# Kernel optimization log

Measured on AMD Instinct MI355X. Metric: run time of the kernel, lower is better.

Reference implementation:

```python
import jax, jax.numpy as jnp
import numpy as np

N = 8192
D_IN = 60
NUM_CLASSES = 10


def _xavier(key, out_f, in_f):
    limit = float(np.sqrt(6.0 / (in_f + out_f)))
    return jax.random.uniform(key, (out_f, in_f), jnp.float32, -limit, limit)


def setup_inputs() -> dict:
    key = jax.random.key(0)
    ks = jax.random.split(key, 10)
    return {
        "x": jax.random.normal(ks[0], (N, D_IN), jnp.float32),
        "fc1_w": _xavier(ks[1], 32, 60),
        "fc1_b": jnp.zeros((32,), jnp.float32),
        "fc2_w": _xavier(ks[2], 16, 32),
        "fc2_b": jnp.zeros((16,), jnp.float32),
        "fc3_w": _xavier(ks[3], 8, 60),
        "fc3_b": jnp.zeros((8,), jnp.float32),
        "fc6_w": _xavier(ks[4], NUM_CLASSES, 8),
        "fc6_b": jnp.zeros((NUM_CLASSES,), jnp.float32),
        "temp": jnp.float32(1.0) + 0.1 * jax.random.truncated_normal(ks[5], -2.0, 2.0, (), jnp.float32),
        "theta": jnp.float32(1.0) + 0.1 * jax.random.truncated_normal(ks[6], -2.0, 2.0, (), jnp.float32),
    }


def _pairwise_sq_dist(z):
    # z: [N, d] -> [N, N] squared euclidean distances, clamped at 0
    sq = jnp.sum(z * z, axis=1)  # [N]
    dist = sq[:, None] + sq[None, :] - 2.0 * (z @ z.T)
    return jnp.maximum(dist, 0.0)


def reference(x, fc1_w, fc1_b, fc2_w, fc2_b, fc3_w, fc3_b, fc6_w, fc6_b, temp, theta):
    net = x @ fc1_w.T + fc1_b           # [N, 32]
    net = net @ fc2_w.T + fc2_b         # [N, 16]
    A = -_pairwise_sq_dist(net)         # [N, N]
    A = jax.nn.sigmoid(temp * A + theta)
    # A * (1 - I) + I == set diagonal to 1
    A = jnp.fill_diagonal(A, 1.0, inplace=False)
    A = A / jnp.sum(A, axis=1, keepdims=True)
    h = A @ x                           # [N, 60] dense graph aggregation
    h = h @ fc3_w.T + fc3_b             # [N, 8]
    return jax.nn.softmax(h @ fc6_w.T + fc6_b, axis=1)  # [N, num_classes]
```

## Files before the change

### kernel.cpp

```cpp
#include <hip/hip_runtime.h>
#include <math.h>

#define NROWS 8192
#define DIN   60
#define DZ    16
#define NC    10

#define LOG2E 1.4426950408889634f

#define RB    64
#define CJ    512
#define NRB   (NROWS / RB)
#define NCH   (NROWS / CJ)
#define WAVES 4

typedef short bf16x8 __attribute__((ext_vector_type(8)));
typedef float f32x4  __attribute__((ext_vector_type(4)));

__device__ __forceinline__ unsigned int bfr(float f) {
    return (__float_as_uint(f) + 0x8000u) >> 16;
}

__global__ __launch_bounds__(64) void k1_all(
    const float* __restrict__ x,
    const float* __restrict__ w1, const float* __restrict__ b1,
    const float* __restrict__ w2, const float* __restrict__ b2,
    const float* __restrict__ temp_p, const float* __restrict__ theta_p,
    unsigned short* __restrict__ zb, float* __restrict__ bbf,
    unsigned short* __restrict__ xT)
{
    int i = blockIdx.x * 64 + threadIdx.x;

    float xr[DIN];
    const float4* xp = reinterpret_cast<const float4*>(x + (size_t)i * DIN);
    #pragma unroll
    for (int c = 0; c < 15; ++c) {
        float4 v = xp[c];
        xr[c*4+0] = v.x; xr[c*4+1] = v.y; xr[c*4+2] = v.z; xr[c*4+3] = v.w;
    }

    float n1[32];
    #pragma unroll
    for (int o = 0; o < 32; ++o) {
        float acc = b1[o];
        #pragma unroll
        for (int k = 0; k < DIN; ++k) acc = fmaf(w1[o*DIN+k], xr[k], acc);
        n1[o] = acc;
    }

    float z[DZ];
    float sq = 0.0f;
    #pragma unroll
    for (int u = 0; u < DZ; ++u) {
        float acc = b2[u];
        #pragma unroll
        for (int o = 0; o < 32; ++o) acc = fmaf(w2[u*32+o], n1[o], acc);
        z[u] = acc;
        sq = fmaf(acc, acc, sq);
    }

    float temp  = *temp_p;
    float theta = *theta_p;
    float s = sqrtf(2.0f * temp * LOG2E);

    unsigned int p[8];
    #pragma unroll
    for (int u = 0; u < 8; ++u) {
        unsigned int lo = bfr(z[2*u]   * s);
        unsigned int hi = bfr(z[2*u+1] * s);
        p[u] = lo | (hi << 16);
    }
    uint4* dst = reinterpret_cast<uint4*>(zb + (size_t)i * 32);
    dst[0] = make_uint4(p[0], p[1], p[2], p[3]);
    dst[1] = make_uint4(p[4], p[5], p[6], p[7]);
    dst[2] = make_uint4(0, 0, 0, 0);
    dst[3] = make_uint4(0, 0, 0, 0);

    bbf[i] = LOG2E * fmaf(temp, sq, -0.5f * theta);

    #pragma unroll
    for (int c = 0; c < DIN; ++c)
        xT[(size_t)c * NROWS + i] = (unsigned short)bfr(xr[c]);
    xT[(size_t)60 * NROWS + i] = 0x3F80;
    xT[(size_t)61 * NROWS + i] = 0;
    xT[(size_t)62 * NROWS + i] = 0;
    xT[(size_t)63 * NROWS + i] = 0;
}

__global__ __launch_bounds__(256, 8) void k2_mfma(
    const unsigned short* __restrict__ zb, const float* __restrict__ bbf,
    const unsigned short* __restrict__ xT, const float* __restrict__ theta_p,
    float* __restrict__ hacc)
{
    __shared__ unsigned long long sP[WAVES * 160];

    const int tid  = threadIdx.x;
    const int lane = tid & 63, wave = tid >> 6;
    const int q = lane & 15, g = lane >> 4;
    const int rb = blockIdx.x & (NRB - 1);
    const int ch = blockIdx.x >> 7;
    const int i0 = rb * RB + wave * 16;
    const int j0 = ch * CJ;

    bf16x8 zbi = *reinterpret_cast<const bf16x8*>(zb + (size_t)(i0 + q) * 32 + g*8);
    float  bi  = bbf[i0 + q];
    const float nclamp = -(*theta_p) * LOG2E;
    const f32x4 z4 = {0.0f, 0.0f, 0.0f, 0.0f};

    f32x4 H[4];
    #pragma unroll
    for (int nt = 0; nt < 4; ++nt) H[nt] = z4;

    unsigned long long* myP = sP + wave * 160;

    for (int jp = 0; jp < CJ / 32; ++jp) {
        #pragma unroll
        for (int half = 0; half < 2; ++half) {
            const int gj = j0 + jp*32 + half*16;
            bf16x8 za = *reinterpret_cast<const bf16x8*>(zb + (size_t)(gj + q) * 32 + g*8);
            f32x4  bj = *reinterpret_cast<const f32x4*>(bbf + gj + 4*g);
            f32x4 S = __builtin_amdgcn_mfma_f32_16x16x32_bf16(za, zbi, z4, 0, 0, 0);
            unsigned int ur[4];
            #pragma unroll
            for (int r = 0; r < 4; ++r) {
                float n = (bi + bj[r]) - S[r];
                n = fmaxf(n, nclamp);
                float P = __builtin_amdgcn_rcpf(1.0f + __builtin_amdgcn_exp2f(n));
                if (i0 == gj && q == 4*g + r) P = 0.0f;
                ur[r] = __float_as_uint(P) + 0x8000u;
            }
            unsigned int pk0 = (ur[0] >> 16) | (ur[1] & 0xFFFF0000u);
            unsigned int pk1 = (ur[2] >> 16) | (ur[3] & 0xFFFF0000u);
            myP[q*10 + half*4 + g] = ((unsigned long long)pk1 << 32) | pk0;
        }
        __threadfence_block();

        const int jb = j0 + jp*32;
        bf16x8 pa;
        {
            union { unsigned long long u[2]; bf16x8 v; } pu;
            pu.u[0] = myP[q*10 + g*2];
            pu.u[1] = myP[q*10 + g*2 + 1];
            pa = pu.v;
        }
        #pragma unroll
        for (int nt = 0; nt < 4; ++nt) {
            bf16x8 xb = *reinterpret_cast<const bf16x8*>(
                xT + (size_t)(nt*16 + q) * NROWS + jb + g*8);
            H[nt] = __builtin_amdgcn_mfma_f32_16x16x32_bf16(pa, xb, H[nt], 0, 0, 0);
        }
    }

    float* regout = hacc + (((size_t)(ch * NRB + rb) * WAVES + wave) * 16) * 64;
    #pragma unroll
    for (int nt = 0; nt < 4; ++nt)
        #pragma unroll
        for (int r = 0; r < 4; ++r)
            regout[(nt*4 + r) * 64 + lane] = H[nt][r];
}

__global__ __launch_bounds__(256) void k3_fused(
    const float* __restrict__ hacc,
    const float* __restrict__ x,
    const float* __restrict__ w3, const float* __restrict__ b3,
    const float* __restrict__ w6, const float* __restrict__ b6,
    float* __restrict__ out)
{
    __shared__ float sh[16][64];

    const int tid = threadIdx.x;
    const int b   = blockIdx.x;

    {
        const float4* src = reinterpret_cast<const float4*>(
            hacc + (size_t)b * 1024) + tid;
        float4 s = make_float4(0.0f, 0.0f, 0.0f, 0.0f);
        #pragma unroll 8
        for (int ch = 0; ch < NCH; ++ch) {
            float4 v = src[(size_t)ch * (NRB * WAVES * 16 * 64 / 4)];
            s.x += v.x; s.y += v.y; s.z += v.z; s.w += v.w;
        }
        const int f    = tid * 4;
        const int lane = f & 63;
        const int slot = (f >> 6) & 15;
        const int il   = (lane >> 4) * 4 + (slot & 3);
        const int cl   = ((slot >> 2) & 3) * 16 + (lane & 15);
        *reinterpret_cast<float4*>(&sh[il][cl]) = s;
    }
    __syncthreads();

    if (tid < 16) {
        const int row = b * 16 + tid;
        const float* hi = sh[tid];
        const float* xi = x + (size_t)row * DIN;

        float rd = __builtin_amdgcn_rcpf(hi[60] + 1.0f);

        float h[DIN];
        #pragma unroll
        for (int k = 0; k < DIN; ++k) h[k] = (hi[k] + xi[k]) * rd;

        float g[8];
        #pragma unroll
        for (int o = 0; o < 8; ++o) {
            float a = b3[o];
            #pragma unroll
            for (int k = 0; k < DIN; ++k) a = fmaf(w3[o*DIN+k], h[k], a);
            g[o] = a;
        }

        float l[NC];
        float m = -3.0e38f;
        #pragma unroll
        for (int c = 0; c < NC; ++c) {
            float a = b6[c];
            #pragma unroll
            for (int o = 0; o < 8; ++o) a = fmaf(w6[c*8+o], g[o], a);
            l[c] = a;
            m = fmaxf(m, a);
        }
        float e[NC];
        float sum = 0.0f;
        #pragma unroll
        for (int c = 0; c < NC; ++c) {
            e[c] = __builtin_amdgcn_exp2f((l[c] - m) * LOG2E);
            sum += e[c];
        }
        float rsum = __builtin_amdgcn_rcpf(sum);
        #pragma unroll
        for (int c = 0; c < NC; ++c) out[(size_t)row * NC + c] = e[c] * rsum;
    }
}

extern "C" void kernel_launch(void* const* d_in, const int* in_sizes, int n_in,
                              void* d_out, int out_size, void* d_ws, size_t ws_size,
                              hipStream_t stream)
{
    const float* x     = (const float*)d_in[0];
    const float* w1    = (const float*)d_in[1];
    const float* b1    = (const float*)d_in[2];
    const float* w2    = (const float*)d_in[3];
    const float* b2    = (const float*)d_in[4];
    const float* w3    = (const float*)d_in[5];
    const float* b3    = (const float*)d_in[6];
    const float* w6    = (const float*)d_in[7];
    const float* b6    = (const float*)d_in[8];
    const float* temp  = (const float*)d_in[9];
    const float* theta = (const float*)d_in[10];
    float* out = (float*)d_out;

    char* p = (char*)d_ws;
    unsigned short* zbuf = (unsigned short*)p;  p += (size_t)NROWS * 32 * 2;
    float*          bbf  = (float*)p;           p += (size_t)NROWS * 4;
    unsigned short* xT   = (unsigned short*)p;  p += (size_t)64 * NROWS * 2;
    float*          hacc = (float*)p;

    k1_all  <<<NROWS / 64, 64, 0, stream>>>(x, w1, b1, w2, b2, temp, theta, zbuf, bbf, xT);
    k2_mfma <<<NRB * NCH, 256, 0, stream>>>(zbuf, bbf, xT, theta, hacc);
    k3_fused<<<NROWS / 16, 256, 0, stream>>>(hacc, x, w3, b3, w6, b6, out);
}
```

Measured before the change: 208.5 us.

## Switch pairwise-similarity kernel to 32x32x16 MFMA with permlane32 register repacking

Moves the distance and aggregation MFMAs from 16x16x32 to 32x32x16 bf16 tiles, with 32 rows per wave and 128 rows per block. The P tile is transposed in registers with permlane32_swap instead of a shared-memory round trip and block fence. The z buffer drops its zero padding from 32 to 16 elements per row. The partial-sum layout is padded per chunk, and k3 is remapped to it with a staggered chunk order. This cuts LDS traffic and raises MFMA work per instruction, in exchange for more accumulator registers and no occupancy hint in launch bounds.

```diff
diff --git a/kernel.cpp b/kernel.cpp
--- a/kernel.cpp
+++ b/kernel.cpp
@@ -8,14 +8,19 @@
 
 #define LOG2E 1.4426950408889634f
 
-#define RB    64
-#define CJ    512
-#define NRB   (NROWS / RB)
-#define NCH   (NROWS / CJ)
-#define WAVES 4
-
-typedef short bf16x8 __attribute__((ext_vector_type(8)));
-typedef float f32x4  __attribute__((ext_vector_type(4)));
+#define RB      128
+#define CJ      512
+#define NRB     (NROWS / RB)
+#define NCH     (NROWS / CJ)
+#define WAVES   4
+#define REGIONS (NRB * WAVES)
+
+#define CHPAD (NROWS * 64 + 1024)
+
+typedef short    bf16x8 __attribute__((ext_vector_type(8)));
+typedef float    f32x4  __attribute__((ext_vector_type(4)));
+typedef float    f32x16 __attribute__((ext_vector_type(16)));
+typedef unsigned u32x2  __attribute__((ext_vector_type(2)));
 
 __device__ __forceinline__ unsigned int bfr(float f) {
     return (__float_as_uint(f) + 0x8000u) >> 16;
@@ -70,11 +75,9 @@
         unsigned int hi = bfr(z[2*u+1] * s);
         p[u] = lo | (hi << 16);
     }
-    uint4* dst = reinterpret_cast<uint4*>(zb + (size_t)i * 32);
+    uint4* dst = reinterpret_cast<uint4*>(zb + (size_t)i * 16);
     dst[0] = make_uint4(p[0], p[1], p[2], p[3]);
     dst[1] = make_uint4(p[4], p[5], p[6], p[7]);
-    dst[2] = make_uint4(0, 0, 0, 0);
-    dst[3] = make_uint4(0, 0, 0, 0);
 
     bbf[i] = LOG2E * fmaf(temp, sq, -0.5f * theta);
 
@@ -87,76 +90,91 @@
     xT[(size_t)63 * NROWS + i] = 0;
 }
 
-__global__ __launch_bounds__(256, 8) void k2_mfma(
+__global__ __launch_bounds__(256) void k2_mfma(
     const unsigned short* __restrict__ zb, const float* __restrict__ bbf,
     const unsigned short* __restrict__ xT, const float* __restrict__ theta_p,
     float* __restrict__ hacc)
 {
-    __shared__ unsigned long long sP[WAVES * 160];
-
     const int tid  = threadIdx.x;
     const int lane = tid & 63, wave = tid >> 6;
-    const int q = lane & 15, g = lane >> 4;
+    const int ic = lane & 31;
+    const int h  = lane >> 5;
     const int rb = blockIdx.x & (NRB - 1);
-    const int ch = blockIdx.x >> 7;
-    const int i0 = rb * RB + wave * 16;
+    const int ch = blockIdx.x >> 6;
+    const int it = rb * RB + wave * 32;
     const int j0 = ch * CJ;
 
-    bf16x8 zbi = *reinterpret_cast<const bf16x8*>(zb + (size_t)(i0 + q) * 32 + g*8);
-    float  bi  = bbf[i0 + q];
+    bf16x8 zbi = *reinterpret_cast<const bf16x8*>(zb + (size_t)(it + ic) * 16 + h * 8);
+    const float bi = bbf[it + ic];
     const float nclamp = -(*theta_p) * LOG2E;
-    const f32x4 z4 = {0.0f, 0.0f, 0.0f, 0.0f};
-
-    f32x4 H[4];
-    #pragma unroll
-    for (int nt = 0; nt < 4; ++nt) H[nt] = z4;
-
-    unsigned long long* myP = sP + wave * 160;
-
-    for (int jp = 0; jp < CJ / 32; ++jp) {
-        #pragma unroll
-        for (int half = 0; half < 2; ++half) {
-            const int gj = j0 + jp*32 + half*16;
-            bf16x8 za = *reinterpret_cast<const bf16x8*>(zb + (size_t)(gj + q) * 32 + g*8);
-            f32x4  bj = *reinterpret_cast<const f32x4*>(bbf + gj + 4*g);
-            f32x4 S = __builtin_amdgcn_mfma_f32_16x16x32_bf16(za, zbi, z4, 0, 0, 0);
-            unsigned int ur[4];
+
+    const int  dd   = ic - 4 * h;
+    const bool dl   = (dd >= 0) && ((dd & 7) < 4);
+    const int  dreg = dl ? (((dd >> 3) << 2) | (dd & 3)) : -1;
+
+    f32x16 z16;
+    #pragma unroll
+    for (int k = 0; k < 16; ++k) z16[k] = 0.0f;
+    f32x16 H0 = z16, H1 = z16;
+
+    for (int jb = 0; jb < CJ / 32; ++jb) {
+        const int jt = j0 + jb * 32;
+        bf16x8 za = *reinterpret_cast<const bf16x8*>(zb + (size_t)(jt + ic) * 16 + h * 8);
+        f32x16 S = __builtin_amdgcn_mfma_f32_32x32x16_bf16(za, zbi, z16, 0, 0, 0);
+
+        const bool dblk = (it == jt);
+        unsigned pk[8];
+        #pragma unroll
+        for (int u = 0; u < 4; ++u) {
+            f32x4 bj = *reinterpret_cast<const f32x4*>(bbf + jt + u * 8 + 4 * h);
+            unsigned ur[4];
             #pragma unroll
             for (int r = 0; r < 4; ++r) {
-                float n = (bi + bj[r]) - S[r];
+                const int reg = u * 4 + r;
+                float n = (bi + bj[r]) - S[reg];
                 n = fmaxf(n, nclamp);
                 float P = __builtin_amdgcn_rcpf(1.0f + __builtin_amdgcn_exp2f(n));
-                if (i0 == gj && q == 4*g + r) P = 0.0f;
+                if (dblk && reg == dreg) P = 0.0f;
                 ur[r] = __float_as_uint(P) + 0x8000u;
             }
-            unsigned int pk0 = (ur[0] >> 16) | (ur[1] & 0xFFFF0000u);
-            unsigned int pk1 = (ur[2] >> 16) | (ur[3] & 0xFFFF0000u);
-            myP[q*10 + half*4 + g] = ((unsigned long long)pk1 << 32) | pk0;
-        }
-        __threadfence_block();
-
-        const int jb = j0 + jp*32;
-        bf16x8 pa;
+            pk[u*2 + 0] = (ur[0] >> 16) | (ur[1] & 0xFFFF0000u);
+            pk[u*2 + 1] = (ur[2] >> 16) | (ur[3] & 0xFFFF0000u);
+        }
+
+        u32x2 sA = __builtin_amdgcn_permlane32_swap(pk[0], pk[2], false, false);
+        u32x2 sB = __builtin_amdgcn_permlane32_swap(pk[1], pk[3], false, false);
+        u32x2 sC = __builtin_amdgcn_permlane32_swap(pk[4], pk[6], false, false);
+        u32x2 sD = __builtin_amdgcn_permlane32_swap(pk[5], pk[7], false, false);
+        union { unsigned u[4]; bf16x8 v; } pa0, pa1;
+        pa0.u[0] = sA[0]; pa0.u[1] = sB[0]; pa0.u[2] = sA[1]; pa0.u[3] = sB[1];
+        pa1.u[0] = sC[0]; pa1.u[1] = sD[0]; pa1.u[2] = sC[1]; pa1.u[3] = sD[1];
+
         {
-            union { unsigned long long u[2]; bf16x8 v; } pu;
-            pu.u[0] = myP[q*10 + g*2];
-            pu.u[1] = myP[q*10 + g*2 + 1];
-            pa = pu.v;
-        }
-        #pragma unroll
-        for (int nt = 0; nt < 4; ++nt) {
-            bf16x8 xb = *reinterpret_cast<const bf16x8*>(
-                xT + (size_t)(nt*16 + q) * NROWS + jb + g*8);
-            H[nt] = __builtin_amdgcn_mfma_f32_16x16x32_bf16(pa, xb, H[nt], 0, 0, 0);
-        }
-    }
-
-    float* regout = hacc + (((size_t)(ch * NRB + rb) * WAVES + wave) * 16) * 64;
-    #pragma unroll
-    for (int nt = 0; nt < 4; ++nt)
-        #pragma unroll
-        for (int r = 0; r < 4; ++r)
-            regout[(nt*4 + r) * 64 + lane] = H[nt][r];
+            bf16x8 xb0 = *reinterpret_cast<const bf16x8*>(
+                xT + (size_t)(ic) * NROWS + jt + h*8);
+            bf16x8 xb1 = *reinterpret_cast<const bf16x8*>(
+                xT + (size_t)(ic) * NROWS + jt + 16 + h*8);
+            H0 = __builtin_amdgcn_mfma_f32_32x32x16_bf16(pa0.v, xb0, H0, 0, 0, 0);
+            H0 = __builtin_amdgcn_mfma_f32_32x32x16_bf16(pa1.v, xb1, H0, 0, 0, 0);
+        }
+        {
+            bf16x8 xb0 = *reinterpret_cast<const bf16x8*>(
+                xT + (size_t)(32 + ic) * NROWS + jt + h*8);
+            bf16x8 xb1 = *reinterpret_cast<const bf16x8*>(
+                xT + (size_t)(32 + ic) * NROWS + jt + 16 + h*8);
+            H1 = __builtin_amdgcn_mfma_f32_32x32x16_bf16(pa0.v, xb0, H1, 0, 0, 0);
+            H1 = __builtin_amdgcn_mfma_f32_32x32x16_bf16(pa1.v, xb1, H1, 0, 0, 0);
+        }
+    }
+
+    const int region = rb * WAVES + wave;
+    float* outp = hacc + (size_t)ch * CHPAD + (size_t)region * 2048;
+    #pragma unroll
+    for (int reg = 0; reg < 16; ++reg)
+        outp[reg * 64 + lane] = H0[reg];
+    #pragma unroll
+    for (int reg = 0; reg < 16; ++reg)
+        outp[(16 + reg) * 64 + lane] = H1[reg];
 }
 
 __global__ __launch_bounds__(256) void k3_fused(
@@ -168,29 +186,33 @@
 {
     __shared__ float sh[16][64];
 
-    const int tid = threadIdx.x;
-    const int b   = blockIdx.x;
+    const int tid    = threadIdx.x;
+    const int b      = blockIdx.x;
+    const int region = b >> 1, sub = b & 1;
 
     {
-        const float4* src = reinterpret_cast<const float4*>(
-            hacc + (size_t)b * 1024) + tid;
+        const int nt   = tid >> 7;
+        const int foff = (tid & 127) * 4;
+        const int rr   = foff >> 6;
+        const int lane = foff & 63;
+        const size_t base = (size_t)region * 2048 + nt * 1024 + sub * 512 + foff;
+
         float4 s = make_float4(0.0f, 0.0f, 0.0f, 0.0f);
-        #pragma unroll 8
-        for (int ch = 0; ch < NCH; ++ch) {
-            float4 v = src[(size_t)ch * (NRB * WAVES * 16 * 64 / 4)];
+        #pragma unroll 4
+        for (int cc = 0; cc < NCH; ++cc) {
+            int ch = (cc + b) & (NCH - 1);
+            float4 v = *reinterpret_cast<const float4*>(
+                hacc + (size_t)ch * CHPAD + base);
             s.x += v.x; s.y += v.y; s.z += v.z; s.w += v.w;
         }
-        const int f    = tid * 4;
-        const int lane = f & 63;
-        const int slot = (f >> 6) & 15;
-        const int il   = (lane >> 4) * 4 + (slot & 3);
-        const int cl   = ((slot >> 2) & 3) * 16 + (lane & 15);
-        *reinterpret_cast<float4*>(&sh[il][cl]) = s;
+        const int il  = (rr & 3) + 8 * (rr >> 2) + 4 * (lane >> 5);
+        const int col = nt * 32 + (lane & 31);
+        *reinterpret_cast<float4*>(&sh[il][col]) = s;
     }
     __syncthreads();
 
     if (tid < 16) {
-        const int row = b * 16 + tid;
+        const int row = region * 32 + sub * 16 + tid;
         const float* hi = sh[tid];
         const float* xi = x + (size_t)row * DIN;
 
@@ -250,12 +272,12 @@
     float* out = (float*)d_out;
 
     char* p = (char*)d_ws;
-    unsigned short* zbuf = (unsigned short*)p;  p += (size_t)NROWS * 32 * 2;
+    unsigned short* zbuf = (unsigned short*)p;  p += (size_t)NROWS * 16 * 2;
     float*          bbf  = (float*)p;           p += (size_t)NROWS * 4;
     unsigned short* xT   = (unsigned short*)p;  p += (size_t)64 * NROWS * 2;
     float*          hacc = (float*)p;
 
     k1_all  <<<NROWS / 64, 64, 0, stream>>>(x, w1, b1, w2, b2, temp, theta, zbuf, bbf, xT);
     k2_mfma <<<NRB * NCH, 256, 0, stream>>>(zbuf, bbf, xT, theta, hacc);
-    k3_fused<<<NROWS / 16, 256, 0, stream>>>(hacc, x, w3, b3, w6, b6, out);
-}
+    k3_fused<<<REGIONS * 2, 256, 0, stream>>>(hacc, x, w3, b3, w6, b6, out);
+}
```

Result: faster. 179.2 us (-14.1%).
